# Kernel tuning notes

Hardware: AMD Instinct MI355X
Metric: run time of the kernel (lower is better)

Reference implementation:

```python
import jax, jax.numpy as jnp
import numpy as np

V = 1_000_000   # sparse_id_num
D = 64          # embedding_dim
F = 26          # sparse_feature_cnt
L = 8           # ids per feature bag (fixed-size ragged regularization)
B = 4096        # batch
IN_DIM = F * D  # 1664
HIDDENS = (1024, 1024, 512)


def setup_inputs() -> dict:
    key = jax.random.key(0)
    ks = jax.random.split(key, 4 + 4 * len(HIDDENS))
    inp = {}
    inp["x"] = jax.random.randint(ks[0], (B, F, L), 0, V, dtype=jnp.int64)
    inp["emb_table"] = jax.random.normal(ks[1], (V, D), dtype=jnp.float32) * 0.01
    ki = 2
    for i, h in enumerate(HIDDENS):
        inp[f"w1_{i}"] = jax.random.normal(ks[ki], (IN_DIM, h), dtype=jnp.float32) * 0.02
        inp[f"b1_{i}"] = jnp.zeros((h,), dtype=jnp.float32)
        inp[f"w2_{i}"] = jax.random.normal(ks[ki + 1], (h, IN_DIM), dtype=jnp.float32) * 0.02
        inp[f"b2_{i}"] = jnp.zeros((IN_DIM,), dtype=jnp.float32)
        ki += 2
    inp["lin_w"] = jax.random.normal(ks[ki], (IN_DIM, 1), dtype=jnp.float32) * 0.02
    inp["lin_b"] = jnp.zeros((1,), dtype=jnp.float32)
    return inp


def reference(x, emb_table,
              w1_0, b1_0, w2_0, b2_0,
              w1_1, b1_1, w2_1, b2_1,
              w1_2, b1_2, w2_2, b2_2,
              lin_w, lin_b):
    # Batched embedding lookup + sum-pool over bag dim + concat over features.
    # x: [B, F, L] -> gather [B, F, L, D] -> sum over L -> [B, F, D] -> [B, F*D]
    pooled = emb_table[x].sum(axis=2)              # [B, F, D]
    feat = pooled.reshape(x.shape[0], -1)          # [B, F*D]
    # Residual blocks: relu(linear2(relu(linear1(x))) + x)
    for w1, b1, w2, b2 in ((w1_0, b1_0, w2_0, b2_0),
                           (w1_1, b1_1, w2_1, b2_1),
                           (w1_2, b1_2, w2_2, b2_2)):
        h = jax.nn.relu(feat @ w1 + b1)
        feat = jax.nn.relu(h @ w2 + b2 + feat)
    return jax.nn.sigmoid(feat @ lin_w + lin_b)    # [B, 1]
```

## Files before the change

kernel.cpp:

```cpp
#include <hip/hip_runtime.h>
#include <hip/hip_bf16.h>

#define BATCH 4096
#define FEATS 26
#define BAG   8
#define EDIM  64
#define INDIM 1664

typedef short bf16x8 __attribute__((ext_vector_type(8)));
typedef float f32x4  __attribute__((ext_vector_type(4)));
typedef unsigned short u16x8 __attribute__((ext_vector_type(8)));

__device__ __forceinline__ unsigned short f2bf(float f) {
    unsigned u = __float_as_uint(f);
    unsigned r = (u + 0x7FFFu + ((u >> 16) & 1u)) >> 16;
    return (unsigned short)r;
}
__device__ __forceinline__ float bf2f(unsigned short h) {
    return __uint_as_float((unsigned)h << 16);
}
__device__ __forceinline__ void async_cp16(const void* g, void* lds_base_uniform) {
    __builtin_amdgcn_global_load_lds(
        (const __attribute__((address_space(1))) unsigned int*)g,
        (__attribute__((address_space(3))) unsigned int*)lds_base_uniform,
        16, 0, 0);
}
#define WAITCNT_VM(n) __builtin_amdgcn_s_waitcnt(0x0F70 | (n))

__global__ __launch_bounds__(256) void transpose_to_bf16(
    const float* __restrict__ in, unsigned short* __restrict__ out, int R, int C)
{
    __shared__ unsigned short tile[64][65];
    const int c0 = blockIdx.x * 64, r0 = blockIdx.y * 64;
    const int t = threadIdx.x;
    const int tc = t & 63, tr = t >> 6;
#pragma unroll
    for (int i = 0; i < 16; ++i) {
        int r = tr + i * 4;
        tile[r][tc] = f2bf(in[(long long)(r0 + r) * C + c0 + tc]);
    }
    __syncthreads();
    const int wr = t >> 3, wc = t & 7;
#pragma unroll
    for (int half = 0; half < 2; ++half) {
        int row = wr + half * 32;
        u16x8 v;
#pragma unroll
        for (int j = 0; j < 8; ++j) v[j] = tile[wc * 8 + j][row];
        *(u16x8*)(out + (long long)(c0 + row) * R + r0 + wc * 8) = v;
    }
}

__global__ __launch_bounds__(256) void embed_pool(
    const int* __restrict__ x, const float* __restrict__ emb,
    unsigned short* __restrict__ feat)
{
    int bag  = blockIdx.x * 4 + (threadIdx.x >> 6);
    int lane = threadIdx.x & 63;
    int b = bag / FEATS;
    int f = bag - b * FEATS;
    const int* xs = x + (long long)bag * BAG;
    float s = 0.f;
#pragma unroll
    for (int l = 0; l < BAG; ++l) {
        int id = xs[l];
        s += emb[(long long)id * EDIM + lane];
    }
    feat[(long long)b * INDIM + f * EDIM + lane] = f2bf(s);
}

#define NBUF 4
__global__ __launch_bounds__(512) void gemm_bf16(
    const unsigned short* __restrict__ A, const unsigned short* __restrict__ Wt,
    const float* __restrict__ bias, const unsigned short* __restrict__ res,
    unsigned short* __restrict__ out, int M, int N, int K, int do_relu)
{
    __shared__ unsigned short As[NBUF * 128 * 32];
    __shared__ unsigned short Bs[NBUF * 128 * 32];

    const int t    = threadIdx.x;
    const int bCol = blockIdx.x * 128;
    const int bRow = blockIdx.y * 128;
    const int wave = t >> 6, lane = t & 63;
    const int wm = wave & 1, wn = wave >> 1;
    const int lm = lane & 15, quad = lane >> 4;

    const int srow = lane >> 2;
    const int sq   = (lane & 3) ^ ((lane >> 3) & 3);
    const unsigned short* Ag = A  + (long long)(bRow + wave * 16 + srow) * K + sq * 8;
    const unsigned short* Bg = Wt + (long long)(bCol + wave * 16 + srow) * K + sq * 8;
    unsigned short* AsW = As + wave * 512;
    unsigned short* BsW = Bs + wave * 512;

    const int T = K / 32;
    f32x4 acc[4][2] = {};

    const int slot = (quad ^ ((lm >> 1) & 3)) * 8;

#define ISSUE(tile_)  do { int _b = (tile_) & (NBUF - 1);                         \
        async_cp16(Ag + (long long)(tile_) * 32, AsW + _b * 4096);                \
        async_cp16(Bg + (long long)(tile_) * 32, BsW + _b * 4096); } while (0)

#define COMPUTE(tile_) do { int _b = (tile_) & (NBUF - 1);                        \
        const unsigned short* _a = As + _b * 4096;                                \
        const unsigned short* _bp = Bs + _b * 4096;                               \
        bf16x8 af[4], bf[2];                                                      \
        _Pragma("unroll")                                                         \
        for (int i = 0; i < 4; ++i)                                               \
            af[i] = *(const bf16x8*)&_a[(wm * 64 + i * 16 + lm) * 32 + slot];     \
        _Pragma("unroll")                                                         \
        for (int j = 0; j < 2; ++j)                                               \
            bf[j] = *(const bf16x8*)&_bp[(wn * 32 + j * 16 + lm) * 32 + slot];    \
        _Pragma("unroll")                                                         \
        for (int i = 0; i < 4; ++i)                                               \
            _Pragma("unroll")                                                     \
            for (int j = 0; j < 2; ++j)                                           \
                acc[i][j] = __builtin_amdgcn_mfma_f32_16x16x32_bf16(              \
                    af[i], bf[j], acc[i][j], 0, 0, 0); } while (0)

    ISSUE(0);
    ISSUE(1);
    for (int tt = 0; tt < T - 2; ++tt) {
        ISSUE(tt + 2);
        WAITCNT_VM(4);
        asm volatile("" ::: "memory");
        __builtin_amdgcn_s_barrier();
        asm volatile("" ::: "memory");
        COMPUTE(tt);
    }
    WAITCNT_VM(2);
    asm volatile("" ::: "memory");
    __builtin_amdgcn_s_barrier();
    asm volatile("" ::: "memory");
    COMPUTE(T - 2);
    WAITCNT_VM(0);
    asm volatile("" ::: "memory");
    __builtin_amdgcn_s_barrier();
    asm volatile("" ::: "memory");
    COMPUTE(T - 1);

#pragma unroll
    for (int i = 0; i < 4; ++i) {
#pragma unroll
        for (int j = 0; j < 2; ++j) {
            int col = bCol + wn * 32 + j * 16 + lm;
            float bv = bias[col];
#pragma unroll
            for (int r = 0; r < 4; ++r) {
                int row = bRow + wm * 64 + i * 16 + quad * 4 + r;
                float v = acc[i][j][r] + bv;
                if (res) v += bf2f(res[(long long)row * N + col]);
                if (do_relu) v = fmaxf(v, 0.f);
                out[(long long)row * N + col] = f2bf(v);
            }
        }
    }
#undef ISSUE
#undef COMPUTE
}

__global__ __launch_bounds__(256) void final_head(
    const unsigned short* __restrict__ feat, const float* __restrict__ lin_w,
    const float* __restrict__ lin_b, float* __restrict__ out)
{
    int row  = blockIdx.x * 4 + (threadIdx.x >> 6);
    int lane = threadIdx.x & 63;
    const unsigned short* fr = feat + (long long)row * INDIM;
    float s = 0.f;
#pragma unroll
    for (int it = 0; it < INDIM / 64; ++it)
        s += bf2f(fr[it * 64 + lane]) * lin_w[it * 64 + lane];
#pragma unroll
    for (int off = 32; off; off >>= 1)
        s += __shfl_down(s, off, 64);
    if (lane == 0)
        out[row] = 1.f / (1.f + __expf(-(s + lin_b[0])));
}

extern "C" void kernel_launch(void* const* d_in, const int* in_sizes, int n_in,
                              void* d_out, int out_size, void* d_ws, size_t ws_size,
                              hipStream_t stream) {
    const int*   x    = (const int*)  d_in[0];
    const float* emb  = (const float*)d_in[1];
    const float* w1_0 = (const float*)d_in[2];
    const float* b1_0 = (const float*)d_in[3];
    const float* w2_0 = (const float*)d_in[4];
    const float* b2_0 = (const float*)d_in[5];
    const float* w1_1 = (const float*)d_in[6];
    const float* b1_1 = (const float*)d_in[7];
    const float* w2_1 = (const float*)d_in[8];
    const float* b2_1 = (const float*)d_in[9];
    const float* w1_2 = (const float*)d_in[10];
    const float* b1_2 = (const float*)d_in[11];
    const float* w2_2 = (const float*)d_in[12];
    const float* b2_2 = (const float*)d_in[13];
    const float* linw = (const float*)d_in[14];
    const float* linb = (const float*)d_in[15];
    float* out = (float*)d_out;

    unsigned short* feat = (unsigned short*)d_ws;
    unsigned short* h    = feat + (long long)BATCH * INDIM;
    unsigned short* p    = h + (long long)BATCH * 1024;
    unsigned short* w1_0t = p; p += 1024 * INDIM;
    unsigned short* w2_0t = p; p += INDIM * 1024;
    unsigned short* w1_1t = p; p += 1024 * INDIM;
    unsigned short* w2_1t = p; p += INDIM * 1024;
    unsigned short* w1_2t = p; p += 512 * INDIM;
    unsigned short* w2_2t = p; p += INDIM * 512;

    transpose_to_bf16<<<dim3(1024/64, INDIM/64), 256, 0, stream>>>(w1_0, w1_0t, INDIM, 1024);
    transpose_to_bf16<<<dim3(INDIM/64, 1024/64), 256, 0, stream>>>(w2_0, w2_0t, 1024, INDIM);
    transpose_to_bf16<<<dim3(1024/64, INDIM/64), 256, 0, stream>>>(w1_1, w1_1t, INDIM, 1024);
    transpose_to_bf16<<<dim3(INDIM/64, 1024/64), 256, 0, stream>>>(w2_1, w2_1t, 1024, INDIM);
    transpose_to_bf16<<<dim3(512/64,  INDIM/64), 256, 0, stream>>>(w1_2, w1_2t, INDIM, 512);
    transpose_to_bf16<<<dim3(INDIM/64, 512/64),  256, 0, stream>>>(w2_2, w2_2t, 512, INDIM);

    embed_pool<<<BATCH * FEATS / 4, 256, 0, stream>>>(x, emb, feat);

    gemm_bf16<<<dim3(1024/128, BATCH/128), 512, 0, stream>>>(
        feat, w1_0t, b1_0, nullptr, h, BATCH, 1024, INDIM, 1);
    gemm_bf16<<<dim3(INDIM/128, BATCH/128), 512, 0, stream>>>(
        h, w2_0t, b2_0, feat, feat, BATCH, INDIM, 1024, 1);
    gemm_bf16<<<dim3(1024/128, BATCH/128), 512, 0, stream>>>(
        feat, w1_1t, b1_1, nullptr, h, BATCH, 1024, INDIM, 1);
    gemm_bf16<<<dim3(INDIM/128, BATCH/128), 512, 0, stream>>>(
        h, w2_1t, b2_1, feat, feat, BATCH, INDIM, 1024, 1);
    gemm_bf16<<<dim3(512/128, BATCH/128), 512, 0, stream>>>(
        feat, w1_2t, b1_2, nullptr, h, BATCH, 512, INDIM, 1);
    gemm_bf16<<<dim3(INDIM/128, BATCH/128), 512, 0, stream>>>(
        h, w2_2t, b2_2, feat, feat, BATCH, INDIM, 512, 1);

    final_head<<<BATCH / 4, 256, 0, stream>>>(feat, linw, linb, out);
}
```

Measured before the change: 568.6 us.

## Shrink GEMM tiles to 64xBN with 256 threads and add XCD-aware block swizzle

```diff
diff --git a/kernel.cpp b/kernel.cpp
--- a/kernel.cpp
+++ b/kernel.cpp
@@ -70,51 +70,67 @@
 }
 
 #define NBUF 4
-__global__ __launch_bounds__(512) void gemm_bf16(
+template<int BN>
+__global__ __launch_bounds__(256, 3) void gemm_bf16(
     const unsigned short* __restrict__ A, const unsigned short* __restrict__ Wt,
     const float* __restrict__ bias, const unsigned short* __restrict__ res,
     unsigned short* __restrict__ out, int M, int N, int K, int do_relu)
 {
-    __shared__ unsigned short As[NBUF * 128 * 32];
-    __shared__ unsigned short Bs[NBUF * 128 * 32];
+    constexpr int JN = BN / 32;
+    constexpr int LT = (BN == 128) ? 3 : 2;
+
+    __shared__ unsigned short As[NBUF * 64 * 32];
+    __shared__ unsigned short Bs[NBUF * BN * 32];
 
     const int t    = threadIdx.x;
-    const int bCol = blockIdx.x * 128;
-    const int bRow = blockIdx.y * 128;
     const int wave = t >> 6, lane = t & 63;
     const int wm = wave & 1, wn = wave >> 1;
     const int lm = lane & 15, quad = lane >> 4;
 
+    const int gx  = gridDim.x;
+    const int nwg = gx << 6;
+    int lin = blockIdx.x * 64 + blockIdx.y;
+    int q = nwg >> 3, r = nwg & 7;
+    int xcd = lin & 7, idx = lin >> 3;
+    int swz = (xcd < r ? xcd * (q + 1) : r * (q + 1) + (xcd - r) * q) + idx;
+    const int bCol = (swz >> 6) * BN;
+    const int bRow = (swz & 63) * 64;
+
     const int srow = lane >> 2;
     const int sq   = (lane & 3) ^ ((lane >> 3) & 3);
-    const unsigned short* Ag = A  + (long long)(bRow + wave * 16 + srow) * K + sq * 8;
-    const unsigned short* Bg = Wt + (long long)(bCol + wave * 16 + srow) * K + sq * 8;
-    unsigned short* AsW = As + wave * 512;
-    unsigned short* BsW = Bs + wave * 512;
+    const unsigned short* Ag  = A  + (long long)(bRow + wave * 16 + srow) * K + sq * 8;
+    const unsigned short* Bg0 = Wt + (long long)(bCol + wave * 16 + srow) * K + sq * 8;
+    const unsigned short* Bg1 = Bg0 + 64 * (long long)K;
+    unsigned short* AsW  = As + wave * 512;
+    unsigned short* BsW0 = Bs + wave * 512;
+    unsigned short* BsW1 = Bs + 2048 + wave * 512;
 
     const int T = K / 32;
-    f32x4 acc[4][2] = {};
+    f32x4 acc[2][JN] = {};
 
     const int slot = (quad ^ ((lm >> 1) & 3)) * 8;
 
 #define ISSUE(tile_)  do { int _b = (tile_) & (NBUF - 1);                         \
-        async_cp16(Ag + (long long)(tile_) * 32, AsW + _b * 4096);                \
-        async_cp16(Bg + (long long)(tile_) * 32, BsW + _b * 4096); } while (0)
+        async_cp16(Ag  + (long long)(tile_) * 32, AsW  + _b * 2048);              \
+        async_cp16(Bg0 + (long long)(tile_) * 32, BsW0 + _b * (BN * 32));         \
+        if constexpr (BN == 128)                                                  \
+            async_cp16(Bg1 + (long long)(tile_) * 32, BsW1 + _b * (BN * 32));     \
+    } while (0)
 
 #define COMPUTE(tile_) do { int _b = (tile_) & (NBUF - 1);                        \
-        const unsigned short* _a = As + _b * 4096;                                \
-        const unsigned short* _bp = Bs + _b * 4096;                               \
-        bf16x8 af[4], bf[2];                                                      \
+        const unsigned short* _a  = As + _b * 2048;                               \
+        const unsigned short* _bp = Bs + _b * (BN * 32);                          \
+        bf16x8 af[2], bf[JN];                                                     \
         _Pragma("unroll")                                                         \
-        for (int i = 0; i < 4; ++i)                                               \
-            af[i] = *(const bf16x8*)&_a[(wm * 64 + i * 16 + lm) * 32 + slot];     \
+        for (int i = 0; i < 2; ++i)                                               \
+            af[i] = *(const bf16x8*)&_a[(wm * 32 + i * 16 + lm) * 32 + slot];     \
         _Pragma("unroll")                                                         \
-        for (int j = 0; j < 2; ++j)                                               \
-            bf[j] = *(const bf16x8*)&_bp[(wn * 32 + j * 16 + lm) * 32 + slot];    \
+        for (int j = 0; j < JN; ++j)                                              \
+            bf[j] = *(const bf16x8*)&_bp[(wn * (BN / 2) + j * 16 + lm) * 32 + slot]; \
         _Pragma("unroll")                                                         \
-        for (int i = 0; i < 4; ++i)                                               \
+        for (int i = 0; i < 2; ++i)                                               \
             _Pragma("unroll")                                                     \
-            for (int j = 0; j < 2; ++j)                                           \
+            for (int j = 0; j < JN; ++j)                                          \
                 acc[i][j] = __builtin_amdgcn_mfma_f32_16x16x32_bf16(              \
                     af[i], bf[j], acc[i][j], 0, 0, 0); } while (0)
 
@@ -122,13 +138,13 @@
     ISSUE(1);
     for (int tt = 0; tt < T - 2; ++tt) {
         ISSUE(tt + 2);
-        WAITCNT_VM(4);
+        WAITCNT_VM(2 * LT);
         asm volatile("" ::: "memory");
         __builtin_amdgcn_s_barrier();
         asm volatile("" ::: "memory");
         COMPUTE(tt);
     }
-    WAITCNT_VM(2);
+    WAITCNT_VM(LT);
     asm volatile("" ::: "memory");
     __builtin_amdgcn_s_barrier();
     asm volatile("" ::: "memory");
@@ -140,15 +156,15 @@
     COMPUTE(T - 1);
 
 #pragma unroll
-    for (int i = 0; i < 4; ++i) {
-#pragma unroll
-        for (int j = 0; j < 2; ++j) {
-            int col = bCol + wn * 32 + j * 16 + lm;
+    for (int i = 0; i < 2; ++i) {
+#pragma unroll
+        for (int j = 0; j < JN; ++j) {
+            int col = bCol + wn * (BN / 2) + j * 16 + lm;
             float bv = bias[col];
 #pragma unroll
-            for (int r = 0; r < 4; ++r) {
-                int row = bRow + wm * 64 + i * 16 + quad * 4 + r;
-                float v = acc[i][j][r] + bv;
+            for (int rr = 0; rr < 4; ++rr) {
+                int row = bRow + wm * 32 + i * 16 + quad * 4 + rr;
+                float v = acc[i][j][rr] + bv;
                 if (res) v += bf2f(res[(long long)row * N + col]);
                 if (do_relu) v = fmaxf(v, 0.f);
                 out[(long long)row * N + col] = f2bf(v);
@@ -217,17 +233,17 @@
 
     embed_pool<<<BATCH * FEATS / 4, 256, 0, stream>>>(x, emb, feat);
 
-    gemm_bf16<<<dim3(1024/128, BATCH/128), 512, 0, stream>>>(
+    gemm_bf16<128><<<dim3(1024/128, BATCH/64), 256, 0, stream>>>(
         feat, w1_0t, b1_0, nullptr, h, BATCH, 1024, INDIM, 1);
-    gemm_bf16<<<dim3(INDIM/128, BATCH/128), 512, 0, stream>>>(
+    gemm_bf16<128><<<dim3(INDIM/128, BATCH/64), 256, 0, stream>>>(
         h, w2_0t, b2_0, feat, feat, BATCH, INDIM, 1024, 1);
-    gemm_bf16<<<dim3(1024/128, BATCH/128), 512, 0, stream>>>(
+    gemm_bf16<128><<<dim3(1024/128, BATCH/64), 256, 0, stream>>>(
         feat, w1_1t, b1_1, nullptr, h, BATCH, 1024, INDIM, 1);
-    gemm_bf16<<<dim3(INDIM/128, BATCH/128), 512, 0, stream>>>(
+    gemm_bf16<128><<<dim3(INDIM/128, BATCH/64), 256, 0, stream>>>(
         h, w2_1t, b2_1, feat, feat, BATCH, INDIM, 1024, 1);
-    gemm_bf16<<<dim3(512/128, BATCH/128), 512, 0, stream>>>(
+    gemm_bf16<64><<<dim3(512/64, BATCH/64), 256, 0, stream>>>(
         feat, w1_2t, b1_2, nullptr, h, BATCH, 512, INDIM, 1);
-    gemm_bf16<<<dim3(INDIM/128, BATCH/128), 512, 0, stream>>>(
+    gemm_bf16<128><<<dim3(INDIM/128, BATCH/64), 256, 0, stream>>>(
         h, w2_2t, b2_2, feat, feat, BATCH, INDIM, 512, 1);
 
     final_head<<<BATCH / 4, 256, 0, stream>>>(feat, linw, linb, out);
```

Result: slower. 582.2 us (+2.4%).

## Fuse MLP GEMM chain into persistent kernel with grid barriers; batch weight transposes

Applied to the files above, without the earlier changes.

```diff
diff --git a/kernel.cpp b/kernel.cpp
--- a/kernel.cpp
+++ b/kernel.cpp
@@ -1,5 +1,4 @@
 #include <hip/hip_runtime.h>
-#include <hip/hip_bf16.h>
 
 #define BATCH 4096
 #define FEATS 26
@@ -27,11 +26,27 @@
 }
 #define WAITCNT_VM(n) __builtin_amdgcn_s_waitcnt(0x0F70 | (n))
 
-__global__ __launch_bounds__(256) void transpose_to_bf16(
-    const float* __restrict__ in, unsigned short* __restrict__ out, int R, int C)
-{
+__global__ __launch_bounds__(256) void transpose_all(
+    const float* __restrict__ w10, unsigned short* __restrict__ o10,
+    const float* __restrict__ w20, unsigned short* __restrict__ o20,
+    const float* __restrict__ w11, unsigned short* __restrict__ o11,
+    const float* __restrict__ w21, unsigned short* __restrict__ o21,
+    const float* __restrict__ w12, unsigned short* __restrict__ o12,
+    const float* __restrict__ w22, unsigned short* __restrict__ o22)
+{
+    const float* in; unsigned short* out; int R, C;
+    switch (blockIdx.z) {
+        case 0:  in = w10; out = o10; R = INDIM; C = 1024;  break;
+        case 1:  in = w20; out = o20; R = 1024;  C = INDIM; break;
+        case 2:  in = w11; out = o11; R = INDIM; C = 1024;  break;
+        case 3:  in = w21; out = o21; R = 1024;  C = INDIM; break;
+        case 4:  in = w12; out = o12; R = INDIM; C = 512;   break;
+        default: in = w22; out = o22; R = 512;   C = INDIM; break;
+    }
+    const int c0 = blockIdx.x * 64, r0 = blockIdx.y * 64;
+    if (c0 >= C || r0 >= R) return;
+
     __shared__ unsigned short tile[64][65];
-    const int c0 = blockIdx.x * 64, r0 = blockIdx.y * 64;
     const int t = threadIdx.x;
     const int tc = t & 63, tr = t >> 6;
 #pragma unroll
@@ -53,8 +68,9 @@
 
 __global__ __launch_bounds__(256) void embed_pool(
     const int* __restrict__ x, const float* __restrict__ emb,
-    unsigned short* __restrict__ feat)
-{
+    unsigned short* __restrict__ feat, unsigned* __restrict__ bar)
+{
+    if (blockIdx.x == 0 && threadIdx.x < 8) bar[threadIdx.x] = 0;
     int bag  = blockIdx.x * 4 + (threadIdx.x >> 6);
     int lane = threadIdx.x & 63;
     int b = bag / FEATS;
@@ -70,32 +86,36 @@
 }
 
 #define NBUF 4
-__global__ __launch_bounds__(512) void gemm_bf16(
-    const unsigned short* __restrict__ A, const unsigned short* __restrict__ Wt,
+
+__device__ void run_stage(
+    unsigned short* As, unsigned short* Bs,
+    const unsigned short* __restrict__ A, const unsigned short* __restrict__ Bt,
     const float* __restrict__ bias, const unsigned short* __restrict__ res,
-    unsigned short* __restrict__ out, int M, int N, int K, int do_relu)
-{
-    __shared__ unsigned short As[NBUF * 128 * 32];
-    __shared__ unsigned short Bs[NBUF * 128 * 32];
-
+    unsigned short* __restrict__ O, int N, int K)
+{
     const int t    = threadIdx.x;
-    const int bCol = blockIdx.x * 128;
-    const int bRow = blockIdx.y * 128;
     const int wave = t >> 6, lane = t & 63;
     const int wm = wave & 1, wn = wave >> 1;
     const int lm = lane & 15, quad = lane >> 4;
-
     const int srow = lane >> 2;
     const int sq   = (lane & 3) ^ ((lane >> 3) & 3);
-    const unsigned short* Ag = A  + (long long)(bRow + wave * 16 + srow) * K + sq * 8;
-    const unsigned short* Bg = Wt + (long long)(bCol + wave * 16 + srow) * K + sq * 8;
-    unsigned short* AsW = As + wave * 512;
-    unsigned short* BsW = Bs + wave * 512;
-
-    const int T = K / 32;
-    f32x4 acc[4][2] = {};
-
     const int slot = (quad ^ ((lm >> 1) & 3)) * 8;
+
+    const int nx = N >> 7;
+    const int nTiles = (BATCH >> 7) * nx;
+    const int T = K >> 5;
+
+    for (int tile = blockIdx.x; tile < nTiles; tile += (int)gridDim.x) {
+        const int trow = tile / nx;
+        const int bRow = trow << 7;
+        const int bCol = (tile - trow * nx) << 7;
+
+        const unsigned short* Ag = A  + (long long)(bRow + wave * 16 + srow) * K + sq * 8;
+        const unsigned short* Bg = Bt + (long long)(bCol + wave * 16 + srow) * K + sq * 8;
+        unsigned short* AsW = As + wave * 512;
+        unsigned short* BsW = Bs + wave * 512;
+
+        f32x4 acc[4][2] = {};
 
 #define ISSUE(tile_)  do { int _b = (tile_) & (NBUF - 1);                         \
         async_cp16(Ag + (long long)(tile_) * 32, AsW + _b * 4096);                \
@@ -118,63 +138,101 @@
                 acc[i][j] = __builtin_amdgcn_mfma_f32_16x16x32_bf16(              \
                     af[i], bf[j], acc[i][j], 0, 0, 0); } while (0)
 
-    ISSUE(0);
-    ISSUE(1);
-    for (int tt = 0; tt < T - 2; ++tt) {
-        ISSUE(tt + 2);
-        WAITCNT_VM(4);
+        ISSUE(0);
+        ISSUE(1);
+        for (int tt = 0; tt < T - 2; ++tt) {
+            ISSUE(tt + 2);
+            WAITCNT_VM(4);
+            asm volatile("" ::: "memory");
+            __builtin_amdgcn_s_barrier();
+            asm volatile("" ::: "memory");
+            COMPUTE(tt);
+        }
+        WAITCNT_VM(2);
         asm volatile("" ::: "memory");
         __builtin_amdgcn_s_barrier();
         asm volatile("" ::: "memory");
-        COMPUTE(tt);
-    }
-    WAITCNT_VM(2);
-    asm volatile("" ::: "memory");
-    __builtin_amdgcn_s_barrier();
-    asm volatile("" ::: "memory");
-    COMPUTE(T - 2);
-    WAITCNT_VM(0);
-    asm volatile("" ::: "memory");
-    __builtin_amdgcn_s_barrier();
-    asm volatile("" ::: "memory");
-    COMPUTE(T - 1);
-
-#pragma unroll
-    for (int i = 0; i < 4; ++i) {
-#pragma unroll
-        for (int j = 0; j < 2; ++j) {
-            int col = bCol + wn * 32 + j * 16 + lm;
-            float bv = bias[col];
-#pragma unroll
-            for (int r = 0; r < 4; ++r) {
-                int row = bRow + wm * 64 + i * 16 + quad * 4 + r;
-                float v = acc[i][j][r] + bv;
-                if (res) v += bf2f(res[(long long)row * N + col]);
-                if (do_relu) v = fmaxf(v, 0.f);
-                out[(long long)row * N + col] = f2bf(v);
+        COMPUTE(T - 2);
+        WAITCNT_VM(0);
+        asm volatile("" ::: "memory");
+        __builtin_amdgcn_s_barrier();
+        asm volatile("" ::: "memory");
+        COMPUTE(T - 1);
+
+#pragma unroll
+        for (int i = 0; i < 4; ++i) {
+#pragma unroll
+            for (int j = 0; j < 2; ++j) {
+                int col = bCol + wn * 32 + j * 16 + lm;
+                float bv = bias[col];
+#pragma unroll
+                for (int rr = 0; rr < 4; ++rr) {
+                    int row = bRow + wm * 64 + i * 16 + quad * 4 + rr;
+                    float v = acc[i][j][rr] + bv;
+                    if (res) v += bf2f(res[(long long)row * N + col]);
+                    v = fmaxf(v, 0.f);
+                    O[(long long)row * N + col] = f2bf(v);
+                }
             }
         }
-    }
 #undef ISSUE
 #undef COMPUTE
-}
-
-__global__ __launch_bounds__(256) void final_head(
-    const unsigned short* __restrict__ feat, const float* __restrict__ lin_w,
-    const float* __restrict__ lin_b, float* __restrict__ out)
-{
-    int row  = blockIdx.x * 4 + (threadIdx.x >> 6);
-    int lane = threadIdx.x & 63;
-    const unsigned short* fr = feat + (long long)row * INDIM;
-    float s = 0.f;
-#pragma unroll
-    for (int it = 0; it < INDIM / 64; ++it)
-        s += bf2f(fr[it * 64 + lane]) * lin_w[it * 64 + lane];
-#pragma unroll
-    for (int off = 32; off; off >>= 1)
-        s += __shfl_down(s, off, 64);
-    if (lane == 0)
-        out[row] = 1.f / (1.f + __expf(-(s + lin_b[0])));
+    }
+}
+
+__device__ __forceinline__ void grid_barrier(unsigned* bar, int slotIdx) {
+    __syncthreads();
+    if (threadIdx.x == 0) {
+        __hip_atomic_fetch_add(&bar[slotIdx], 1u, __ATOMIC_ACQ_REL,
+                               __HIP_MEMORY_SCOPE_AGENT);
+        while (__hip_atomic_load(&bar[slotIdx], __ATOMIC_ACQUIRE,
+                                 __HIP_MEMORY_SCOPE_AGENT) < gridDim.x)
+            __builtin_amdgcn_s_sleep(8);
+    }
+    __syncthreads();
+}
+
+__global__ __launch_bounds__(512, 4) void mlp_chain(
+    unsigned short* __restrict__ feat, unsigned short* __restrict__ h,
+    const unsigned short* __restrict__ w10t, const float* __restrict__ b10,
+    const unsigned short* __restrict__ w20t, const float* __restrict__ b20,
+    const unsigned short* __restrict__ w11t, const float* __restrict__ b11,
+    const unsigned short* __restrict__ w21t, const float* __restrict__ b21,
+    const unsigned short* __restrict__ w12t, const float* __restrict__ b12,
+    const unsigned short* __restrict__ w22t, const float* __restrict__ b22,
+    const float* __restrict__ linw, const float* __restrict__ linb,
+    float* __restrict__ out, unsigned* bar)
+{
+    __shared__ unsigned short As[NBUF * 128 * 32];
+    __shared__ unsigned short Bs[NBUF * 128 * 32];
+
+    run_stage(As, Bs, feat, w10t, b10, nullptr, h,    1024,  INDIM);
+    grid_barrier(bar, 0);
+    run_stage(As, Bs, h,    w20t, b20, feat,    feat, INDIM, 1024);
+    grid_barrier(bar, 1);
+    run_stage(As, Bs, feat, w11t, b11, nullptr, h,    1024,  INDIM);
+    grid_barrier(bar, 2);
+    run_stage(As, Bs, h,    w21t, b21, feat,    feat, INDIM, 1024);
+    grid_barrier(bar, 3);
+    run_stage(As, Bs, feat, w12t, b12, nullptr, h,    512,   INDIM);
+    grid_barrier(bar, 4);
+    run_stage(As, Bs, h,    w22t, b22, feat,    feat, INDIM, 512);
+    grid_barrier(bar, 5);
+
+    const int wave = threadIdx.x >> 6, lane = threadIdx.x & 63;
+    int row = blockIdx.x * 8 + wave;
+    if (row < BATCH) {
+        const unsigned short* fr = feat + (long long)row * INDIM;
+        float s = 0.f;
+#pragma unroll
+        for (int it = 0; it < INDIM / 64; ++it)
+            s += bf2f(fr[it * 64 + lane]) * linw[it * 64 + lane];
+#pragma unroll
+        for (int off = 32; off; off >>= 1)
+            s += __shfl_down(s, off, 64);
+        if (lane == 0)
+            out[row] = 1.f / (1.f + __expf(-(s + linb[0])));
+    }
 }
 
 extern "C" void kernel_launch(void* const* d_in, const int* in_sizes, int n_in,
@@ -207,28 +265,14 @@
     unsigned short* w2_1t = p; p += INDIM * 1024;
     unsigned short* w1_2t = p; p += 512 * INDIM;
     unsigned short* w2_2t = p; p += INDIM * 512;
-
-    transpose_to_bf16<<<dim3(1024/64, INDIM/64), 256, 0, stream>>>(w1_0, w1_0t, INDIM, 1024);
-    transpose_to_bf16<<<dim3(INDIM/64, 1024/64), 256, 0, stream>>>(w2_0, w2_0t, 1024, INDIM);
-    transpose_to_bf16<<<dim3(1024/64, INDIM/64), 256, 0, stream>>>(w1_1, w1_1t, INDIM, 1024);
-    transpose_to_bf16<<<dim3(INDIM/64, 1024/64), 256, 0, stream>>>(w2_1, w2_1t, 1024, INDIM);
-    transpose_to_bf16<<<dim3(512/64,  INDIM/64), 256, 0, stream>>>(w1_2, w1_2t, INDIM, 512);
-    transpose_to_bf16<<<dim3(INDIM/64, 512/64),  256, 0, stream>>>(w2_2, w2_2t, 512, INDIM);
-
-    embed_pool<<<BATCH * FEATS / 4, 256, 0, stream>>>(x, emb, feat);
-
-    gemm_bf16<<<dim3(1024/128, BATCH/128), 512, 0, stream>>>(
-        feat, w1_0t, b1_0, nullptr, h, BATCH, 1024, INDIM, 1);
-    gemm_bf16<<<dim3(INDIM/128, BATCH/128), 512, 0, stream>>>(
-        h, w2_0t, b2_0, feat, feat, BATCH, INDIM, 1024, 1);
-    gemm_bf16<<<dim3(1024/128, BATCH/128), 512, 0, stream>>>(
-        feat, w1_1t, b1_1, nullptr, h, BATCH, 1024, INDIM, 1);
-    gemm_bf16<<<dim3(INDIM/128, BATCH/128), 512, 0, stream>>>(
-        h, w2_1t, b2_1, feat, feat, BATCH, INDIM, 1024, 1);
-    gemm_bf16<<<dim3(512/128, BATCH/128), 512, 0, stream>>>(
-        feat, w1_2t, b1_2, nullptr, h, BATCH, 512, INDIM, 1);
-    gemm_bf16<<<dim3(INDIM/128, BATCH/128), 512, 0, stream>>>(
-        h, w2_2t, b2_2, feat, feat, BATCH, INDIM, 512, 1);
-
-    final_head<<<BATCH / 4, 256, 0, stream>>>(feat, linw, linb, out);
-}
+    unsigned*       bar   = (unsigned*)p;
+
+    transpose_all<<<dim3(26, 26, 6), 256, 0, stream>>>(
+        w1_0, w1_0t, w2_0, w2_0t, w1_1, w1_1t, w2_1, w2_1t, w1_2, w1_2t, w2_2, w2_2t);
+
+    embed_pool<<<BATCH * FEATS / 4, 256, 0, stream>>>(x, emb, feat, bar);
+
+    mlp_chain<<<512, 512, 0, stream>>>(
+        feat, h, w1_0t, b1_0, w2_0t, b2_0, w1_1t, b1_1, w2_1t, b2_1,
+        w1_2t, b1_2, w2_2t, b2_2, linw, linb, out, bar);
+}
```

New measurement: 1.512 ms. +166.0%, slower.

## Sort embedding lookups by id bucket and accumulate with atomics; merge weight transposes

Applied to the files above, without the earlier changes.

```diff
diff --git a/kernel.cpp b/kernel.cpp
--- a/kernel.cpp
+++ b/kernel.cpp
@@ -1,11 +1,12 @@
 #include <hip/hip_runtime.h>
-#include <hip/hip_bf16.h>
 
 #define BATCH 4096
 #define FEATS 26
 #define BAG   8
 #define EDIM  64
 #define INDIM 1664
+#define NENT  (BATCH * FEATS * BAG)
+#define NBUCK 1024
 
 typedef short bf16x8 __attribute__((ext_vector_type(8)));
 typedef float f32x4  __attribute__((ext_vector_type(4)));
@@ -27,11 +28,27 @@
 }
 #define WAITCNT_VM(n) __builtin_amdgcn_s_waitcnt(0x0F70 | (n))
 
-__global__ __launch_bounds__(256) void transpose_to_bf16(
-    const float* __restrict__ in, unsigned short* __restrict__ out, int R, int C)
-{
+__global__ __launch_bounds__(256) void transpose_all(
+    const float* __restrict__ w10, unsigned short* __restrict__ o10,
+    const float* __restrict__ w20, unsigned short* __restrict__ o20,
+    const float* __restrict__ w11, unsigned short* __restrict__ o11,
+    const float* __restrict__ w21, unsigned short* __restrict__ o21,
+    const float* __restrict__ w12, unsigned short* __restrict__ o12,
+    const float* __restrict__ w22, unsigned short* __restrict__ o22)
+{
+    const float* in; unsigned short* out; int R, C;
+    switch (blockIdx.z) {
+        case 0:  in = w10; out = o10; R = INDIM; C = 1024;  break;
+        case 1:  in = w20; out = o20; R = 1024;  C = INDIM; break;
+        case 2:  in = w11; out = o11; R = INDIM; C = 1024;  break;
+        case 3:  in = w21; out = o21; R = 1024;  C = INDIM; break;
+        case 4:  in = w12; out = o12; R = INDIM; C = 512;   break;
+        default: in = w22; out = o22; R = 512;   C = INDIM; break;
+    }
+    const int c0 = blockIdx.x * 64, r0 = blockIdx.y * 64;
+    if (c0 >= C || r0 >= R) return;
+
     __shared__ unsigned short tile[64][65];
-    const int c0 = blockIdx.x * 64, r0 = blockIdx.y * 64;
     const int t = threadIdx.x;
     const int tc = t & 63, tr = t >> 6;
 #pragma unroll
@@ -51,22 +68,79 @@
     }
 }
 
-__global__ __launch_bounds__(256) void embed_pool(
-    const int* __restrict__ x, const float* __restrict__ emb,
-    unsigned short* __restrict__ feat)
-{
-    int bag  = blockIdx.x * 4 + (threadIdx.x >> 6);
-    int lane = threadIdx.x & 63;
-    int b = bag / FEATS;
-    int f = bag - b * FEATS;
-    const int* xs = x + (long long)bag * BAG;
-    float s = 0.f;
-#pragma unroll
-    for (int l = 0; l < BAG; ++l) {
-        int id = xs[l];
-        s += emb[(long long)id * EDIM + lane];
-    }
-    feat[(long long)b * INDIM + f * EDIM + lane] = f2bf(s);
+__global__ __launch_bounds__(256) void zero_pooled(
+    float* __restrict__ pooled, unsigned* __restrict__ cnts )
+{
+    int i = blockIdx.x * 256 + threadIdx.x;
+    *(f32x4*)(pooled + (long long)i * 4) = (f32x4){0.f, 0.f, 0.f, 0.f};
+    if (i < 2 * NBUCK) cnts[i] = 0;
+}
+
+__global__ __launch_bounds__(256) void hist_ids(
+    const int* __restrict__ x, unsigned* __restrict__ cnt)
+{
+    __shared__ unsigned lc[NBUCK];
+    for (int i = threadIdx.x; i < NBUCK; i += 256) lc[i] = 0;
+    __syncthreads();
+    for (int i = blockIdx.x * 256 + threadIdx.x; i < NENT; i += gridDim.x * 256)
+        atomicAdd(&lc[((unsigned)x[i]) >> 10], 1u);
+    __syncthreads();
+    for (int i = threadIdx.x; i < NBUCK; i += 256)
+        if (lc[i]) atomicAdd(&cnt[i], lc[i]);
+}
+
+__global__ __launch_bounds__(64) void scan_buckets(
+    const unsigned* __restrict__ cnt, unsigned* __restrict__ cur)
+{
+    const int lane = threadIdx.x;
+    unsigned v[16], s = 0;
+#pragma unroll
+    for (int j = 0; j < 16; ++j) { v[j] = cnt[lane * 16 + j]; s += v[j]; }
+    unsigned incl = s;
+#pragma unroll
+    for (int off = 1; off < 64; off <<= 1) {
+        unsigned t = __shfl_up(incl, off, 64);
+        if (lane >= off) incl += t;
+    }
+    unsigned run = incl - s;
+#pragma unroll
+    for (int j = 0; j < 16; ++j) { cur[lane * 16 + j] = run; run += v[j]; }
+}
+
+__global__ __launch_bounds__(256) void scatter_ids(
+    const int* __restrict__ x, unsigned* __restrict__ cur, uint2* __restrict__ srt)
+{
+    for (int i = blockIdx.x * 256 + threadIdx.x; i < NENT; i += gridDim.x * 256) {
+        unsigned id = (unsigned)x[i];
+        unsigned slot = atomicAdd(&cur[id >> 10], 1u);
+        srt[slot] = make_uint2(id, (unsigned)(i >> 3));
+    }
+}
+
+__global__ __launch_bounds__(256) void gather_accum(
+    const uint2* __restrict__ srt, const float* __restrict__ emb,
+    float* __restrict__ pooled)
+{
+    const int nw   = (gridDim.x * 256) >> 6;
+    const int w    = (blockIdx.x * 256 + threadIdx.x) >> 6;
+    const int lane = threadIdx.x & 63;
+    for (int e = w; e < NENT; e += nw) {
+        uint2 s = srt[e];
+        float v = emb[(long long)s.x * EDIM + lane];
+        unsafeAtomicAdd(&pooled[(long long)s.y * EDIM + lane], v);
+    }
+}
+
+__global__ __launch_bounds__(256) void convert_feat(
+    const float* __restrict__ pooled, unsigned short* __restrict__ feat)
+{
+    int i = blockIdx.x * 256 + threadIdx.x;
+    f32x4 a = *(const f32x4*)(pooled + (long long)i * 8);
+    f32x4 b = *(const f32x4*)(pooled + (long long)i * 8 + 4);
+    u16x8 o;
+#pragma unroll
+    for (int j = 0; j < 4; ++j) { o[j] = f2bf(a[j]); o[j + 4] = f2bf(b[j]); }
+    *(u16x8*)(feat + (long long)i * 8) = o;
 }
 
 #define NBUF 4
@@ -94,7 +168,6 @@
 
     const int T = K / 32;
     f32x4 acc[4][2] = {};
-
     const int slot = (quad ^ ((lm >> 1) & 3)) * 8;
 
 #define ISSUE(tile_)  do { int _b = (tile_) & (NBUF - 1);                         \
@@ -207,15 +280,21 @@
     unsigned short* w2_1t = p; p += INDIM * 1024;
     unsigned short* w1_2t = p; p += 512 * INDIM;
     unsigned short* w2_2t = p; p += INDIM * 512;
-
-    transpose_to_bf16<<<dim3(1024/64, INDIM/64), 256, 0, stream>>>(w1_0, w1_0t, INDIM, 1024);
-    transpose_to_bf16<<<dim3(INDIM/64, 1024/64), 256, 0, stream>>>(w2_0, w2_0t, 1024, INDIM);
-    transpose_to_bf16<<<dim3(1024/64, INDIM/64), 256, 0, stream>>>(w1_1, w1_1t, INDIM, 1024);
-    transpose_to_bf16<<<dim3(INDIM/64, 1024/64), 256, 0, stream>>>(w2_1, w2_1t, 1024, INDIM);
-    transpose_to_bf16<<<dim3(512/64,  INDIM/64), 256, 0, stream>>>(w1_2, w1_2t, INDIM, 512);
-    transpose_to_bf16<<<dim3(INDIM/64, 512/64),  256, 0, stream>>>(w2_2, w2_2t, 512, INDIM);
-
-    embed_pool<<<BATCH * FEATS / 4, 256, 0, stream>>>(x, emb, feat);
+    float*  pooled = (float*)p;
+    uint2*  srt    = (uint2*)(pooled + (long long)BATCH * INDIM);
+    unsigned* cnts = (unsigned*)(srt + NENT);
+    unsigned* cnt  = cnts;
+    unsigned* cur  = cnts + NBUCK;
+
+    transpose_all<<<dim3(26, 26, 6), 256, 0, stream>>>(
+        w1_0, w1_0t, w2_0, w2_0t, w1_1, w1_1t, w2_1, w2_1t, w1_2, w1_2t, w2_2, w2_2t);
+
+    zero_pooled<<<(BATCH * INDIM / 4) / 256, 256, 0, stream>>>(pooled, cnts);
+    hist_ids<<<256, 256, 0, stream>>>(x, cnt);
+    scan_buckets<<<1, 64, 0, stream>>>(cnt, cur);
+    scatter_ids<<<1024, 256, 0, stream>>>(x, cur, srt);
+    gather_accum<<<4096, 256, 0, stream>>>(srt, emb, pooled);
+    convert_feat<<<(NENT) / 256, 256, 0, stream>>>(pooled, feat);
 
     gemm_bf16<<<dim3(1024/128, BATCH/128), 512, 0, stream>>>(
         feat, w1_0t, b1_0, nullptr, h, BATCH, 1024, INDIM, 1);
```

Result: slower. 878.5 us (+54.5%).
